# Kernel optimization log

Measured on AMD Instinct MI355X. Metric: run time of the kernel, lower is better.

## Reference

```python
import jax, jax.numpy as jnp
import numpy as np
from jax import lax

C = 256          # in_channels
CM = 16          # mid_channels = C // reduction_factor
BS = 8           # attention block size
NG = 32          # GroupNorm groups
EPS = 1e-5


def _dw(x, w, b):
    # depthwise 3x3, padding=1 -> SAME; kernel w: (C, 1, 3, 3)
    y = lax.conv_general_dilated(x, w, (1, 1), 'SAME',
                                 dimension_numbers=('NCHW', 'OIHW', 'NCHW'),
                                 feature_group_count=x.shape[1])
    return y + b[None, :, None, None]


def _pw(x, w, b):
    # pointwise 1x1 conv; w: (O, C)
    return jnp.einsum('bchw,oc->bohw', x, w) + b[None, :, None, None]


def _blocks(x, hb, wb):
    # (B, Cc, H, W) -> (B*hb*wb, Cc, BS*BS)
    B, Cc, H, W = x.shape
    x = x.reshape(B, Cc, hb, BS, wb, BS).transpose(0, 2, 4, 1, 3, 5)
    return x.reshape(B * hb * wb, Cc, BS * BS)


def _attention(q_src, k_src, v_src, p):
    B, Cin, H, W = q_src.shape
    q = _pw(_dw(q_src, p['qdw_w'], p['qdw_b']), p['qpw_w'], p['qpw_b'])  # (B,CM,H,W)
    k = _pw(_dw(k_src, p['kdw_w'], p['kdw_b']), p['kpw_w'], p['kpw_b'])  # (B,CM,H,W)
    v = _pw(_dw(v_src, p['vdw_w'], p['vdw_b']), p['vpw_w'], p['vpw_b'])  # (B,C,H,W)
    hb, wb = H // BS, W // BS  # H,W chosen divisible by BS (pad path is no-op)
    qb = _blocks(q, hb, wb)
    kb = _blocks(k, hb, wb)
    vb = _blocks(v, hb, wb)
    attn = jax.nn.softmax(jnp.einsum('ncp,ncq->npq', qb, kb) / (CM ** 0.5), axis=-1)
    out = jnp.einsum('ncq,npq->ncp', vb, attn)  # (N, C, 64)
    out = out.reshape(B, hb, wb, Cin, BS, BS).transpose(0, 3, 1, 4, 2, 5)
    return out.reshape(B, Cin, H, W)


def _group_norm(x, gamma, beta):
    B, Cc, H, W = x.shape
    xg = x.reshape(B, NG, Cc // NG, H, W)
    mu = jnp.mean(xg, axis=(2, 3, 4), keepdims=True)
    var = jnp.var(xg, axis=(2, 3, 4), keepdims=True)
    xg = (xg - mu) * lax.rsqrt(var + EPS)
    x = xg.reshape(B, Cc, H, W)
    return x * gamma[None, :, None, None] + beta[None, :, None, None]


def setup_inputs() -> dict:
    key = jax.random.key(0)
    ks = jax.random.split(key, 12)
    s = 0.05
    return {
        'img_feat': jax.random.normal(ks[0], (8, C, 128, 128), jnp.float32),
        'mask_feat': jax.random.normal(ks[1], (8, C, 128, 128), jnp.float32),
        'qdw_w': jax.random.normal(ks[2], (C, 1, 3, 3), jnp.float32) * s,
        'qdw_b': jnp.zeros((C,), jnp.float32),
        'kdw_w': jax.random.normal(ks[3], (C, 1, 3, 3), jnp.float32) * s,
        'kdw_b': jnp.zeros((C,), jnp.float32),
        'vdw_w': jax.random.normal(ks[4], (C, 1, 3, 3), jnp.float32) * s,
        'vdw_b': jnp.zeros((C,), jnp.float32),
        'qpw_w': jax.random.normal(ks[5], (CM, C), jnp.float32) * s,
        'qpw_b': jnp.zeros((CM,), jnp.float32),
        'kpw_w': jax.random.normal(ks[6], (CM, C), jnp.float32) * s,
        'kpw_b': jnp.zeros((CM,), jnp.float32),
        'vpw_w': jax.random.normal(ks[7], (C, C), jnp.float32) * s,
        'vpw_b': jnp.zeros((C,), jnp.float32),
        'alpha': jnp.float32(0.5),
        'beta': jnp.float32(0.5),
        'gn_w': jnp.ones((C,), jnp.float32),
        'gn_b': jnp.zeros((C,), jnp.float32),
    }


def reference(img_feat, mask_feat, qdw_w, qdw_b, kdw_w, kdw_b, vdw_w, vdw_b,
              qpw_w, qpw_b, kpw_w, kpw_b, vpw_w, vpw_b, alpha, beta, gn_w, gn_b):
    p = dict(qdw_w=qdw_w, qdw_b=qdw_b, kdw_w=kdw_w, kdw_b=kdw_b,
             vdw_w=vdw_w, vdw_b=vdw_b, qpw_w=qpw_w, qpw_b=qpw_b,
             kpw_w=kpw_w, kpw_b=kpw_b, vpw_w=vpw_w, vpw_b=vpw_b)
    mask_enhanced = _attention(mask_feat, img_feat, img_feat, p)
    img_enhanced = _attention(img_feat, mask_feat, mask_feat, p)
    fused = alpha * mask_enhanced + beta * img_enhanced + img_feat + mask_feat
    return _group_norm(fused, gn_w, gn_b)
```

## Files before the change

kernel.cpp:

```cpp
#include <hip/hip_runtime.h>
#include <hip/hip_bf16.h>

using bf16 = __hip_bfloat16;

typedef short s16x8 __attribute__((ext_vector_type(8)));
typedef float f32x4 __attribute__((ext_vector_type(4)));

#define TPB 512
#define MFMA16(a, b, c) __builtin_amdgcn_mfma_f32_16x16x32_bf16((a), (b), (c), 0, 0, 0)

__device__ __forceinline__ float b2f(bf16 h) { return __bfloat162float(h); }
__device__ __forceinline__ bf16  f2b(float f) { return __float2bfloat16(f); }
__device__ __forceinline__ void unpack2(unsigned int v, float& lo, float& hi) {
  lo = __builtin_bit_cast(float, v << 16);
  hi = __builtin_bit_cast(float, v & 0xffff0000u);
}
__device__ __forceinline__ void unpack8(uint4 u, float* f) {
  unpack2(u.x, f[0], f[1]); unpack2(u.y, f[2], f[3]);
  unpack2(u.z, f[4], f[5]); unpack2(u.w, f[6], f[7]);
}
__device__ __forceinline__ unsigned int pack2(float a, float b) {
  unsigned int lo = (unsigned int)__builtin_bit_cast(unsigned short, __float2bfloat16(a));
  unsigned int hi = (unsigned int)__builtin_bit_cast(unsigned short, __float2bfloat16(b));
  return lo | (hi << 16);
}
__device__ __forceinline__ s16x8 cvt8(float4 a, float4 b) {
  uint4 u;
  u.x = pack2(a.x, a.y); u.y = pack2(a.z, a.w);
  u.z = pack2(b.x, b.y); u.w = pack2(b.z, b.w);
  return __builtin_bit_cast(s16x8, u);
}

struct __align__(16) SMem {
  bf16 patch[256 * 100];
  union {
    bf16 dwT[64 * 264];
    bf16 vA[256 * 72];
    bf16 outT[256 * 72];
  } R1;
  bf16 R2[256 * 72];
  bf16 probs1[64 * 72];
  bf16 probs2[64 * 72];
  bf16 q1[16 * 64];
  bf16 k1[16 * 64];
  bf16 q2[16 * 64];
  bf16 k2[16 * 64];
  float red[2 * 8 * 64];
  float stats[64];
};

__device__ __forceinline__ void load_patch(SMem& sm, const float* __restrict__ src,
                                           int b, int by, int bx, int tid) {
  const int gx4 = bx * 8;
  for (int u = tid; u < 2560; u += TPB) {
    int c = u / 10, py = u - c * 10;
    int gy = by * 8 + py - 1;
    unsigned int* d32 = (unsigned int*)&sm.patch[c * 100 + py * 10];
    if (gy < 0 || gy > 127) {
      #pragma unroll
      for (int i = 0; i < 5; i++) d32[i] = 0u;
      continue;
    }
    const float* srow = src + (((long long)(b * 256 + c)) << 14) + ((long long)gy << 7);
    float4 t1 = *(const float4*)(srow + gx4);
    float4 t2 = *(const float4*)(srow + gx4 + 4);
    float first = (bx > 0) ? srow[gx4 - 1] : 0.0f;
    float last  = (bx < 15) ? srow[gx4 + 8] : 0.0f;
    d32[0] = pack2(first, t1.x);
    d32[1] = pack2(t1.y, t1.z);
    d32[2] = pack2(t1.w, t2.x);
    d32[3] = pack2(t2.y, t2.z);
    d32[4] = pack2(t2.w, last);
  }
}

__device__ __forceinline__ void load_prow(const bf16* p, float* r) {
  const unsigned int* q = (const unsigned int*)p;
  #pragma unroll
  for (int i = 0; i < 5; i++) unpack2(q[i], r[2 * i], r[2 * i + 1]);
}

__device__ __forceinline__ void dw_phase(SMem& sm, const float* __restrict__ w9,
                                         const float* __restrict__ bias, int tid) {
  int c = tid & 255, h = tid >> 8;
  float wr[9];
  #pragma unroll
  for (int i = 0; i < 9; i++) wr[i] = w9[c * 9 + i];
  float bs = bias[c];
  const bf16* prow = &sm.patch[c * 100];
  float r0[10], r1[10], r2[10];
  load_prow(prow + (4 * h) * 10, r0);
  load_prow(prow + (4 * h + 1) * 10, r1);
  bf16* dst = sm.R1.dwT;
  #pragma unroll
  for (int t = 0; t < 4; t++) {
    int ly = 4 * h + t;
    load_prow(prow + (ly + 2) * 10, r2);
    #pragma unroll
    for (int lx = 0; lx < 8; lx++) {
      float a = bs
        + r0[lx] * wr[0] + r0[lx + 1] * wr[1] + r0[lx + 2] * wr[2]
        + r1[lx] * wr[3] + r1[lx + 1] * wr[4] + r1[lx + 2] * wr[5]
        + r2[lx] * wr[6] + r2[lx + 1] * wr[7] + r2[lx + 2] * wr[8];
      dst[(ly * 8 + lx) * 264 + c] = f2b(a);
    }
    #pragma unroll
    for (int i = 0; i < 10; i++) { r0[i] = r1[i]; r1[i] = r2[i]; }
  }
}

__device__ __forceinline__ void pw_qk(SMem& sm, const float* __restrict__ w,
                                      const float* __restrict__ bias, bf16* dst,
                                      float scale, int tid) {
  int p = tid & 63, og = tid >> 6;
  const bf16* dwp = &sm.R1.dwT[p * 264];
  float acc0 = 0.f, acc1 = 0.f;
  #pragma unroll 4
  for (int c0 = 0; c0 < 256; c0 += 8) {
    uint4 du = *(const uint4*)(dwp + c0);
    float d[8]; unpack8(du, d);
    const float* w0 = w + og * 256 + c0;
    const float* w1 = w + (og + 8) * 256 + c0;
    float4 w0a = *(const float4*)w0, w0b = *(const float4*)(w0 + 4);
    float4 w1a = *(const float4*)w1, w1b = *(const float4*)(w1 + 4);
    acc0 += w0a.x * d[0] + w0a.y * d[1] + w0a.z * d[2] + w0a.w * d[3]
          + w0b.x * d[4] + w0b.y * d[5] + w0b.z * d[6] + w0b.w * d[7];
    acc1 += w1a.x * d[0] + w1a.y * d[1] + w1a.z * d[2] + w1a.w * d[3]
          + w1b.x * d[4] + w1b.y * d[5] + w1b.z * d[6] + w1b.w * d[7];
  }
  dst[og * 64 + p]       = f2b(scale * (acc0 + bias[og]));
  dst[(og + 8) * 64 + p] = f2b(scale * (acc1 + bias[og + 8]));
}

__device__ __forceinline__ void scores_softmax(SMem& sm, const bf16* q, const bf16* k,
                                               bf16* probs, int tid) {
  int p = tid & 63, rq = tid >> 6;
  int r0 = rq * 8;
  float s[8] = {0, 0, 0, 0, 0, 0, 0, 0};
  #pragma unroll 4
  for (int o = 0; o < 16; o++) {
    float qv = b2f(q[o * 64 + p]);
    uint4 ku = *(const uint4*)(k + o * 64 + r0);
    float kf[8]; unpack8(ku, kf);
    #pragma unroll
    for (int j = 0; j < 8; j++) s[j] += qv * kf[j];
  }
  float m = s[0];
  #pragma unroll
  for (int j = 1; j < 8; j++) m = fmaxf(m, s[j]);
  sm.red[rq * 64 + p] = m;
  __syncthreads();
  float M = sm.red[p];
  #pragma unroll
  for (int j = 1; j < 8; j++) M = fmaxf(M, sm.red[j * 64 + p]);
  float e[8], sum = 0.f;
  #pragma unroll
  for (int j = 0; j < 8; j++) { e[j] = __expf(s[j] - M); sum += e[j]; }
  sm.red[512 + rq * 64 + p] = sum;
  __syncthreads();
  float S = 0.f;
  #pragma unroll
  for (int j = 0; j < 8; j++) S += sm.red[512 + j * 64 + p];
  float inv = 1.0f / S;
  uint4 pk;
  pk.x = pack2(e[0] * inv, e[1] * inv);
  pk.y = pack2(e[2] * inv, e[3] * inv);
  pk.z = pack2(e[4] * inv, e[5] * inv);
  pk.w = pack2(e[6] * inv, e[7] * inv);
  *(uint4*)(probs + p * 72 + r0) = pk;
}

__device__ __forceinline__ void vgemm(SMem& sm, const float* __restrict__ vpw,
                                      const float* __restrict__ vpb, bf16* dstVA,
                                      float scale, int tid) {
  int lane = tid & 63, wv = tid >> 6;
  int quad = lane >> 4, l16 = lane & 15;
  int m0 = wv * 2;
  f32x4 acc[2][4];
  #pragma unroll
  for (int a = 0; a < 2; a++)
    #pragma unroll
    for (int n = 0; n < 4; n++) acc[a][n] = (f32x4){0.f, 0.f, 0.f, 0.f};
  const bf16* dwT = sm.R1.dwT;
  #pragma unroll 2
  for (int kt = 0; kt < 8; kt++) {
    int k0 = kt * 32 + quad * 8;
    const float* ar0 = vpw + (m0 * 16 + l16) * 256 + k0;
    const float* ar1 = vpw + ((m0 + 1) * 16 + l16) * 256 + k0;
    s16x8 a0 = cvt8(*(const float4*)ar0, *(const float4*)(ar0 + 4));
    s16x8 a1 = cvt8(*(const float4*)ar1, *(const float4*)(ar1 + 4));
    s16x8 bF[4];
    #pragma unroll
    for (int n = 0; n < 4; n++)
      bF[n] = __builtin_bit_cast(s16x8, *(const uint4*)(dwT + (n * 16 + l16) * 264 + k0));
    #pragma unroll
    for (int n = 0; n < 4; n++) {
      acc[0][n] = MFMA16(a0, bF[n], acc[0][n]);
      acc[1][n] = MFMA16(a1, bF[n], acc[1][n]);
    }
  }
  __syncthreads();
  #pragma unroll
  for (int a = 0; a < 2; a++) {
    #pragma unroll
    for (int i = 0; i < 4; i++) {
      int c = (m0 + a) * 16 + quad * 4 + i;
      float bs = vpb[c];
      #pragma unroll
      for (int n = 0; n < 4; n++) {
        int r = n * 16 + l16;
        dstVA[c * 72 + r] = f2b(scale * (acc[a][n][i] + bs));
      }
    }
  }
}

__device__ __forceinline__ void ogemm(const bf16* __restrict__ vA, const bf16* __restrict__ probs,
                                      f32x4 acc[2][4], int tid) {
  int lane = tid & 63, wv = tid >> 6;
  int quad = lane >> 4, l16 = lane & 15;
  int m0 = wv * 2;
  #pragma unroll
  for (int kt = 0; kt < 2; kt++) {
    int k0 = kt * 32 + quad * 8;
    s16x8 a0 = __builtin_bit_cast(s16x8, *(const uint4*)(vA + (m0 * 16 + l16) * 72 + k0));
    s16x8 a1 = __builtin_bit_cast(s16x8, *(const uint4*)(vA + ((m0 + 1) * 16 + l16) * 72 + k0));
    #pragma unroll
    for (int n = 0; n < 4; n++) {
      s16x8 bF = __builtin_bit_cast(s16x8, *(const uint4*)(probs + (n * 16 + l16) * 72 + k0));
      acc[0][n] = MFMA16(a0, bF, acc[0][n]);
      acc[1][n] = MFMA16(a1, bF, acc[1][n]);
    }
  }
}

__device__ __forceinline__ void add_center(SMem& sm, f32x4 acc[2][4], int tid) {
  int lane = tid & 63, wv = tid >> 6, quad = lane >> 4, l16 = lane & 15;
  int m0 = wv * 2;
  #pragma unroll
  for (int a = 0; a < 2; a++)
    #pragma unroll
    for (int i = 0; i < 4; i++) {
      int c = (m0 + a) * 16 + quad * 4 + i;
      const bf16* prow = &sm.patch[c * 100];
      #pragma unroll
      for (int n = 0; n < 4; n++) {
        int p = n * 16 + l16;
        int ly = p >> 3, lx = p & 7;
        acc[a][n][i] += b2f(prow[(ly + 1) * 10 + (lx + 1)]);
      }
    }
}

__global__ __launch_bounds__(TPB, 2) void bicaf_main(
    const float* __restrict__ img, const float* __restrict__ msk,
    const float* __restrict__ qdw_w, const float* __restrict__ qdw_b,
    const float* __restrict__ kdw_w, const float* __restrict__ kdw_b,
    const float* __restrict__ vdw_w, const float* __restrict__ vdw_b,
    const float* __restrict__ qpw_w, const float* __restrict__ qpw_b,
    const float* __restrict__ kpw_w, const float* __restrict__ kpw_b,
    const float* __restrict__ vpw_w, const float* __restrict__ vpw_b,
    const float* __restrict__ alphap, const float* __restrict__ betap,
    float* __restrict__ out, float* __restrict__ gstats) {
  __shared__ SMem sm;
  int tid = threadIdx.x;
  int i = blockIdx.x;
  int bx = (i >> 3) & 15;
  int gi = (i & 7) | ((i >> 7) << 3);
  int b = gi >> 4, by = gi & 15;

  if (tid < 64) sm.stats[tid] = 0.f;
  float alpha = alphap[0], beta = betap[0];

  load_patch(sm, img, b, by, bx, tid);
  __syncthreads();
  dw_phase(sm, qdw_w, qdw_b, tid); __syncthreads();
  pw_qk(sm, qpw_w, qpw_b, sm.q2, 0.25f, tid); __syncthreads();
  dw_phase(sm, kdw_w, kdw_b, tid); __syncthreads();
  pw_qk(sm, kpw_w, kpw_b, sm.k1, 1.0f, tid); __syncthreads();
  dw_phase(sm, vdw_w, vdw_b, tid); __syncthreads();
  vgemm(sm, vpw_w, vpw_b, sm.R2, alpha, tid);

  f32x4 facc[2][4];
  #pragma unroll
  for (int a = 0; a < 2; a++)
    #pragma unroll
    for (int n = 0; n < 4; n++) facc[a][n] = (f32x4){0.f, 0.f, 0.f, 0.f};
  add_center(sm, facc, tid);
  __syncthreads();

  load_patch(sm, msk, b, by, bx, tid);
  __syncthreads();
  dw_phase(sm, qdw_w, qdw_b, tid); __syncthreads();
  pw_qk(sm, qpw_w, qpw_b, sm.q1, 0.25f, tid); __syncthreads();
  dw_phase(sm, kdw_w, kdw_b, tid); __syncthreads();
  pw_qk(sm, kpw_w, kpw_b, sm.k2, 1.0f, tid); __syncthreads();
  dw_phase(sm, vdw_w, vdw_b, tid); __syncthreads();
  vgemm(sm, vpw_w, vpw_b, sm.R1.vA, beta, tid);
  __syncthreads();
  scores_softmax(sm, sm.q1, sm.k1, sm.probs1, tid); __syncthreads();
  scores_softmax(sm, sm.q2, sm.k2, sm.probs2, tid); __syncthreads();
  ogemm(sm.R1.vA, sm.probs2, facc, tid);
  ogemm(sm.R2, sm.probs1, facc, tid);
  add_center(sm, facc, tid);

  {
    int lane = tid & 63, wv = tid >> 6, quad = lane >> 4;
    int m0 = wv * 2;
    #pragma unroll
    for (int a = 0; a < 2; a++) {
      int g = (((m0 + a) * 16 + quad * 4) >> 3);
      float s = 0.f, ss = 0.f;
      #pragma unroll
      for (int n = 0; n < 4; n++)
        #pragma unroll
        for (int ii = 0; ii < 4; ii++) { float v = facc[a][n][ii]; s += v; ss += v * v; }
      atomicAdd(&sm.stats[g * 2], s);
      atomicAdd(&sm.stats[g * 2 + 1], ss);
    }
  }
  __syncthreads();

  {
    int lane = tid & 63, wv = tid >> 6, quad = lane >> 4, l16 = lane & 15;
    int m0 = wv * 2;
    #pragma unroll
    for (int a = 0; a < 2; a++)
      #pragma unroll
      for (int ii = 0; ii < 4; ii++) {
        int c = (m0 + a) * 16 + quad * 4 + ii;
        #pragma unroll
        for (int n = 0; n < 4; n++)
          sm.R1.outT[c * 72 + n * 16 + l16] = f2b(facc[a][n][ii]);
      }
  }
  __syncthreads();

  if (tid < 64) atomicAdd(&gstats[b * 64 + tid], sm.stats[tid]);

  {
    int c = tid & 255, h = tid >> 8;
    float* obase = out + (((long long)(b * 256 + c)) << 14) + (long long)(by * 8) * 128 + bx * 8;
    #pragma unroll
    for (int t = 0; t < 4; t++) {
      int ly = 4 * h + t;
      uint4 v = *(const uint4*)&sm.R1.outT[c * 72 + ly * 8];
      float f[8]; unpack8(v, f);
      *(float4*)(obase + ly * 128)     = make_float4(f[0], f[1], f[2], f[3]);
      *(float4*)(obase + ly * 128 + 4) = make_float4(f[4], f[5], f[6], f[7]);
    }
  }
}

__global__ __launch_bounds__(256) void gn_apply(float* __restrict__ out,
    const float* __restrict__ gstats, const float* __restrict__ gw,
    const float* __restrict__ gb) {
  long long idx = ((long long)blockIdx.x * 256 + threadIdx.x) * 8;
  int c = (int)((idx >> 14) & 255);
  int b = (int)(idx >> 22);
  int g = c >> 3;
  float sum = gstats[b * 64 + g * 2], ss = gstats[b * 64 + g * 2 + 1];
  const float inv_n = 1.0f / 131072.0f;
  float mean = sum * inv_n;
  float var = ss * inv_n - mean * mean;
  float rstd = rsqrtf(var + 1e-5f);
  float sc = gw[c] * rstd;
  float sh = gb[c] - mean * sc;
  float4 v0 = *(const float4*)(out + idx);
  float4 v1 = *(const float4*)(out + idx + 4);
  v0.x = v0.x * sc + sh; v0.y = v0.y * sc + sh;
  v0.z = v0.z * sc + sh; v0.w = v0.w * sc + sh;
  v1.x = v1.x * sc + sh; v1.y = v1.y * sc + sh;
  v1.z = v1.z * sc + sh; v1.w = v1.w * sc + sh;
  *(float4*)(out + idx) = v0;
  *(float4*)(out + idx + 4) = v1;
}

extern "C" void kernel_launch(void* const* d_in, const int* in_sizes, int n_in,
                              void* d_out, int out_size, void* d_ws, size_t ws_size,
                              hipStream_t stream) {
  (void)in_sizes; (void)n_in; (void)out_size; (void)ws_size;
  const float* img    = (const float*)d_in[0];
  const float* msk    = (const float*)d_in[1];
  const float* qdw_w  = (const float*)d_in[2];
  const float* qdw_b  = (const float*)d_in[3];
  const float* kdw_w  = (const float*)d_in[4];
  const float* kdw_b  = (const float*)d_in[5];
  const float* vdw_w  = (const float*)d_in[6];
  const float* vdw_b  = (const float*)d_in[7];
  const float* qpw_w  = (const float*)d_in[8];
  const float* qpw_b  = (const float*)d_in[9];
  const float* kpw_w  = (const float*)d_in[10];
  const float* kpw_b  = (const float*)d_in[11];
  const float* vpw_w  = (const float*)d_in[12];
  const float* vpw_b  = (const float*)d_in[13];
  const float* alphap = (const float*)d_in[14];
  const float* betap  = (const float*)d_in[15];
  const float* gn_w   = (const float*)d_in[16];
  const float* gn_b   = (const float*)d_in[17];
  float* out = (float*)d_out;
  float* gstats = (float*)d_ws;

  hipMemsetAsync(d_ws, 0, 2048, stream);
  bicaf_main<<<dim3(2048), dim3(TPB), 0, stream>>>(
      img, msk, qdw_w, qdw_b, kdw_w, kdw_b, vdw_w, vdw_b,
      qpw_w, qpw_b, kpw_w, kpw_b, vpw_w, vpw_b, alphap, betap, out, gstats);
  gn_apply<<<dim3(16384), dim3(256), 0, stream>>>(out, gstats, gn_w, gn_b);
}
```

Before: 972.7 us.

## Fuse GroupNorm apply into main kernel via cooperative grid sync and register stash

```diff
diff --git a/kernel.cpp b/kernel.cpp
--- a/kernel.cpp
+++ b/kernel.cpp
@@ -1,5 +1,8 @@
 #include <hip/hip_runtime.h>
 #include <hip/hip_bf16.h>
+#include <hip/hip_cooperative_groups.h>
+
+namespace cg = cooperative_groups;
 
 using bf16 = __hip_bfloat16;
 
@@ -112,7 +115,8 @@
 __device__ __forceinline__ void pw_qk(SMem& sm, const float* __restrict__ w,
                                       const float* __restrict__ bias, bf16* dst,
                                       float scale, int tid) {
-  int p = tid & 63, og = tid >> 6;
+  int p = tid & 63;
+  int og = __builtin_amdgcn_readfirstlane(tid >> 6);
   const bf16* dwp = &sm.R1.dwT[p * 264];
   float acc0 = 0.f, acc1 = 0.f;
   #pragma unroll 4
@@ -173,7 +177,8 @@
 __device__ __forceinline__ void vgemm(SMem& sm, const float* __restrict__ vpw,
                                       const float* __restrict__ vpb, bf16* dstVA,
                                       float scale, int tid) {
-  int lane = tid & 63, wv = tid >> 6;
+  int lane = tid & 63;
+  int wv = __builtin_amdgcn_readfirstlane(tid >> 6);
   int quad = lane >> 4, l16 = lane & 15;
   int m0 = wv * 2;
   f32x4 acc[2][4];
@@ -217,7 +222,8 @@
 
 __device__ __forceinline__ void ogemm(const bf16* __restrict__ vA, const bf16* __restrict__ probs,
                                       f32x4 acc[2][4], int tid) {
-  int lane = tid & 63, wv = tid >> 6;
+  int lane = tid & 63;
+  int wv = __builtin_amdgcn_readfirstlane(tid >> 6);
   int quad = lane >> 4, l16 = lane & 15;
   int m0 = wv * 2;
   #pragma unroll
@@ -252,7 +258,7 @@
     }
 }
 
-__global__ __launch_bounds__(TPB, 2) void bicaf_main(
+__global__ __launch_bounds__(TPB, 2) void bicaf_fused(
     const float* __restrict__ img, const float* __restrict__ msk,
     const float* __restrict__ qdw_w, const float* __restrict__ qdw_b,
     const float* __restrict__ kdw_w, const float* __restrict__ kdw_b,
@@ -261,119 +267,142 @@
     const float* __restrict__ kpw_w, const float* __restrict__ kpw_b,
     const float* __restrict__ vpw_w, const float* __restrict__ vpw_b,
     const float* __restrict__ alphap, const float* __restrict__ betap,
+    const float* __restrict__ gw, const float* __restrict__ gb,
     float* __restrict__ out, float* __restrict__ gstats) {
   __shared__ SMem sm;
   int tid = threadIdx.x;
-  int i = blockIdx.x;
-  int bx = (i >> 3) & 15;
-  int gi = (i & 7) | ((i >> 7) << 3);
-  int b = gi >> 4, by = gi & 15;
-
-  if (tid < 64) sm.stats[tid] = 0.f;
+  int j = blockIdx.x;
   float alpha = alphap[0], beta = betap[0];
 
-  load_patch(sm, img, b, by, bx, tid);
-  __syncthreads();
-  dw_phase(sm, qdw_w, qdw_b, tid); __syncthreads();
-  pw_qk(sm, qpw_w, qpw_b, sm.q2, 0.25f, tid); __syncthreads();
-  dw_phase(sm, kdw_w, kdw_b, tid); __syncthreads();
-  pw_qk(sm, kpw_w, kpw_b, sm.k1, 1.0f, tid); __syncthreads();
-  dw_phase(sm, vdw_w, vdw_b, tid); __syncthreads();
-  vgemm(sm, vpw_w, vpw_b, sm.R2, alpha, tid);
-
-  f32x4 facc[2][4];
-  #pragma unroll
-  for (int a = 0; a < 2; a++)
-    #pragma unroll
-    for (int n = 0; n < 4; n++) facc[a][n] = (f32x4){0.f, 0.f, 0.f, 0.f};
-  add_center(sm, facc, tid);
-  __syncthreads();
-
-  load_patch(sm, msk, b, by, bx, tid);
-  __syncthreads();
-  dw_phase(sm, qdw_w, qdw_b, tid); __syncthreads();
-  pw_qk(sm, qpw_w, qpw_b, sm.q1, 0.25f, tid); __syncthreads();
-  dw_phase(sm, kdw_w, kdw_b, tid); __syncthreads();
-  pw_qk(sm, kpw_w, kpw_b, sm.k2, 1.0f, tid); __syncthreads();
-  dw_phase(sm, vdw_w, vdw_b, tid); __syncthreads();
-  vgemm(sm, vpw_w, vpw_b, sm.R1.vA, beta, tid);
-  __syncthreads();
-  scores_softmax(sm, sm.q1, sm.k1, sm.probs1, tid); __syncthreads();
-  scores_softmax(sm, sm.q2, sm.k2, sm.probs2, tid); __syncthreads();
-  ogemm(sm.R1.vA, sm.probs2, facc, tid);
-  ogemm(sm.R2, sm.probs1, facc, tid);
-  add_center(sm, facc, tid);
+  unsigned int stash[8][16];
+
+  #pragma unroll 1
+  for (int t = 0; t < 8; ++t) {
+    int i = j + (t << 8);
+    int bx = (i >> 3) & 15;
+    int gi = (i & 7) | ((i >> 7) << 3);
+    int b = gi >> 4, by = gi & 15;
+
+    if (tid < 64) sm.stats[tid] = 0.f;
+
+    load_patch(sm, img, b, by, bx, tid);
+    __syncthreads();
+    dw_phase(sm, qdw_w, qdw_b, tid); __syncthreads();
+    pw_qk(sm, qpw_w, qpw_b, sm.q2, 0.25f, tid); __syncthreads();
+    dw_phase(sm, kdw_w, kdw_b, tid); __syncthreads();
+    pw_qk(sm, kpw_w, kpw_b, sm.k1, 1.0f, tid); __syncthreads();
+    dw_phase(sm, vdw_w, vdw_b, tid); __syncthreads();
+    vgemm(sm, vpw_w, vpw_b, sm.R2, alpha, tid);
+
+    f32x4 facc[2][4];
+    #pragma unroll
+    for (int a = 0; a < 2; a++)
+      #pragma unroll
+      for (int n = 0; n < 4; n++) facc[a][n] = (f32x4){0.f, 0.f, 0.f, 0.f};
+    add_center(sm, facc, tid);
+    __syncthreads();
+
+    load_patch(sm, msk, b, by, bx, tid);
+    __syncthreads();
+    dw_phase(sm, qdw_w, qdw_b, tid); __syncthreads();
+    pw_qk(sm, qpw_w, qpw_b, sm.q1, 0.25f, tid); __syncthreads();
+    dw_phase(sm, kdw_w, kdw_b, tid); __syncthreads();
+    pw_qk(sm, kpw_w, kpw_b, sm.k2, 1.0f, tid); __syncthreads();
+    dw_phase(sm, vdw_w, vdw_b, tid); __syncthreads();
+    vgemm(sm, vpw_w, vpw_b, sm.R1.vA, beta, tid);
+    __syncthreads();
+    scores_softmax(sm, sm.q1, sm.k1, sm.probs1, tid); __syncthreads();
+    scores_softmax(sm, sm.q2, sm.k2, sm.probs2, tid); __syncthreads();
+    ogemm(sm.R1.vA, sm.probs2, facc, tid);
+    ogemm(sm.R2, sm.probs1, facc, tid);
+    add_center(sm, facc, tid);
+
+    {
+      int lane = tid & 63, wv = tid >> 6, quad = lane >> 4;
+      int m0 = wv * 2;
+      #pragma unroll
+      for (int a = 0; a < 2; a++) {
+        int g = (((m0 + a) * 16 + quad * 4) >> 3);
+        float s = 0.f, ss = 0.f;
+        #pragma unroll
+        for (int n = 0; n < 4; n++)
+          #pragma unroll
+          for (int ii = 0; ii < 4; ii++) { float v = facc[a][n][ii]; s += v; ss += v * v; }
+        atomicAdd(&sm.stats[g * 2], s);
+        atomicAdd(&sm.stats[g * 2 + 1], ss);
+      }
+    }
+    __syncthreads();
+
+    if (tid < 64) atomicAdd(&gstats[b * 64 + tid], sm.stats[tid]);
+
+    #pragma unroll
+    for (int a = 0; a < 2; a++)
+      #pragma unroll
+      for (int n = 0; n < 4; n++) {
+        stash[t][a * 8 + n * 2 + 0] = pack2(facc[a][n][0], facc[a][n][1]);
+        stash[t][a * 8 + n * 2 + 1] = pack2(facc[a][n][2], facc[a][n][3]);
+      }
+  }
+
+  cg::this_grid().sync();
 
   {
-    int lane = tid & 63, wv = tid >> 6, quad = lane >> 4;
-    int m0 = wv * 2;
-    #pragma unroll
-    for (int a = 0; a < 2; a++) {
-      int g = (((m0 + a) * 16 + quad * 4) >> 3);
-      float s = 0.f, ss = 0.f;
-      #pragma unroll
-      for (int n = 0; n < 4; n++)
-        #pragma unroll
-        for (int ii = 0; ii < 4; ii++) { float v = facc[a][n][ii]; s += v; ss += v * v; }
-      atomicAdd(&sm.stats[g * 2], s);
-      atomicAdd(&sm.stats[g * 2 + 1], ss);
-    }
-  }
-  __syncthreads();
-
-  {
+    int c = tid & 255, h = tid >> 8;
+    float gwc = gw[c], gbc = gb[c];
     int lane = tid & 63, wv = tid >> 6, quad = lane >> 4, l16 = lane & 15;
     int m0 = wv * 2;
-    #pragma unroll
-    for (int a = 0; a < 2; a++)
-      #pragma unroll
-      for (int ii = 0; ii < 4; ii++) {
-        int c = (m0 + a) * 16 + quad * 4 + ii;
+
+    #pragma unroll 1
+    for (int t = 0; t < 8; ++t) {
+      int i = j + (t << 8);
+      int bx = (i >> 3) & 15;
+      int gi = (i & 7) | ((i >> 7) << 3);
+      int b = gi >> 4, by = gi & 15;
+
+      {
+        unsigned short* oT = (unsigned short*)sm.R1.outT;
         #pragma unroll
-        for (int n = 0; n < 4; n++)
-          sm.R1.outT[c * 72 + n * 16 + l16] = f2b(facc[a][n][ii]);
-      }
-  }
-  __syncthreads();
-
-  if (tid < 64) atomicAdd(&gstats[b * 64 + tid], sm.stats[tid]);
-
-  {
-    int c = tid & 255, h = tid >> 8;
-    float* obase = out + (((long long)(b * 256 + c)) << 14) + (long long)(by * 8) * 128 + bx * 8;
-    #pragma unroll
-    for (int t = 0; t < 4; t++) {
-      int ly = 4 * h + t;
-      uint4 v = *(const uint4*)&sm.R1.outT[c * 72 + ly * 8];
-      float f[8]; unpack8(v, f);
-      *(float4*)(obase + ly * 128)     = make_float4(f[0], f[1], f[2], f[3]);
-      *(float4*)(obase + ly * 128 + 4) = make_float4(f[4], f[5], f[6], f[7]);
-    }
-  }
-}
-
-__global__ __launch_bounds__(256) void gn_apply(float* __restrict__ out,
-    const float* __restrict__ gstats, const float* __restrict__ gw,
-    const float* __restrict__ gb) {
-  long long idx = ((long long)blockIdx.x * 256 + threadIdx.x) * 8;
-  int c = (int)((idx >> 14) & 255);
-  int b = (int)(idx >> 22);
-  int g = c >> 3;
-  float sum = gstats[b * 64 + g * 2], ss = gstats[b * 64 + g * 2 + 1];
-  const float inv_n = 1.0f / 131072.0f;
-  float mean = sum * inv_n;
-  float var = ss * inv_n - mean * mean;
-  float rstd = rsqrtf(var + 1e-5f);
-  float sc = gw[c] * rstd;
-  float sh = gb[c] - mean * sc;
-  float4 v0 = *(const float4*)(out + idx);
-  float4 v1 = *(const float4*)(out + idx + 4);
-  v0.x = v0.x * sc + sh; v0.y = v0.y * sc + sh;
-  v0.z = v0.z * sc + sh; v0.w = v0.w * sc + sh;
-  v1.x = v1.x * sc + sh; v1.y = v1.y * sc + sh;
-  v1.z = v1.z * sc + sh; v1.w = v1.w * sc + sh;
-  *(float4*)(out + idx) = v0;
-  *(float4*)(out + idx + 4) = v1;
+        for (int a = 0; a < 2; a++) {
+          int cb = (m0 + a) * 16 + quad * 4;
+          #pragma unroll
+          for (int n = 0; n < 4; n++) {
+            unsigned int d0 = stash[t][a * 8 + n * 2];
+            unsigned int d1 = stash[t][a * 8 + n * 2 + 1];
+            int col = n * 16 + l16;
+            oT[(cb + 0) * 72 + col] = (unsigned short)(d0 & 0xffffu);
+            oT[(cb + 1) * 72 + col] = (unsigned short)(d0 >> 16);
+            oT[(cb + 2) * 72 + col] = (unsigned short)(d1 & 0xffffu);
+            oT[(cb + 3) * 72 + col] = (unsigned short)(d1 >> 16);
+          }
+        }
+      }
+      __syncthreads();
+
+      {
+        int g = c >> 3;
+        float sum = gstats[b * 64 + g * 2], ssum = gstats[b * 64 + g * 2 + 1];
+        const float inv_n = 1.0f / 131072.0f;
+        float mean = sum * inv_n;
+        float var = ssum * inv_n - mean * mean;
+        float rstd = rsqrtf(var + 1e-5f);
+        float scl = gwc * rstd;
+        float sh = gbc - mean * scl;
+        float* obase = out + (((long long)(b * 256 + c)) << 14) + (long long)(by * 8) * 128 + bx * 8;
+        #pragma unroll
+        for (int r4 = 0; r4 < 4; r4++) {
+          int ly = 4 * h + r4;
+          uint4 v = *(const uint4*)&sm.R1.outT[c * 72 + ly * 8];
+          float f[8]; unpack8(v, f);
+          #pragma unroll
+          for (int q = 0; q < 8; q++) f[q] = f[q] * scl + sh;
+          *(float4*)(obase + ly * 128)     = make_float4(f[0], f[1], f[2], f[3]);
+          *(float4*)(obase + ly * 128 + 4) = make_float4(f[4], f[5], f[6], f[7]);
+        }
+      }
+      __syncthreads();
+    }
+  }
 }
 
 extern "C" void kernel_launch(void* const* d_in, const int* in_sizes, int n_in,
@@ -402,8 +431,13 @@
   float* gstats = (float*)d_ws;
 
   hipMemsetAsync(d_ws, 0, 2048, stream);
-  bicaf_main<<<dim3(2048), dim3(TPB), 0, stream>>>(
-      img, msk, qdw_w, qdw_b, kdw_w, kdw_b, vdw_w, vdw_b,
-      qpw_w, qpw_b, kpw_w, kpw_b, vpw_w, vpw_b, alphap, betap, out, gstats);
-  gn_apply<<<dim3(16384), dim3(256), 0, stream>>>(out, gstats, gn_w, gn_b);
-}
+  void* args[] = {
+    (void*)&img, (void*)&msk, (void*)&qdw_w, (void*)&qdw_b,
+    (void*)&kdw_w, (void*)&kdw_b, (void*)&vdw_w, (void*)&vdw_b,
+    (void*)&qpw_w, (void*)&qpw_b, (void*)&kpw_w, (void*)&kpw_b,
+    (void*)&vpw_w, (void*)&vpw_b, (void*)&alphap, (void*)&betap,
+    (void*)&gn_w, (void*)&gn_b, (void*)&out, (void*)&gstats
+  };
+  hipLaunchCooperativeKernel(reinterpret_cast<void*>(bicaf_fused),
+                             dim3(256), dim3(TPB), args, 0, stream);
+}
```

After: 933.1 us. 4.1% less time.

## Halve patch LDS footprint, keep V fragments in registers, persistent 4-tile blocks

Applied to the files above, without the earlier changes.

```diff
diff --git a/kernel.cpp b/kernel.cpp
--- a/kernel.cpp
+++ b/kernel.cpp
@@ -32,15 +32,15 @@
 }
 
 struct __align__(16) SMem {
-  bf16 patch[256 * 100];
+  union {
+    bf16 patchH[128 * 100];
+    struct { bf16 probs1[64 * 72]; bf16 probs2[64 * 72]; } P;
+  } U0;
   union {
     bf16 dwT[64 * 264];
     bf16 vA[256 * 72];
     bf16 outT[256 * 72];
   } R1;
-  bf16 R2[256 * 72];
-  bf16 probs1[64 * 72];
-  bf16 probs2[64 * 72];
   bf16 q1[16 * 64];
   bf16 k1[16 * 64];
   bf16 q2[16 * 64];
@@ -49,19 +49,20 @@
   float stats[64];
 };
 
-__device__ __forceinline__ void load_patch(SMem& sm, const float* __restrict__ src,
-                                           int b, int by, int bx, int tid) {
+__device__ __forceinline__ void load_patch_h(SMem& sm, const float* __restrict__ src,
+                                             int b, int by, int bx, int half, int tid) {
   const int gx4 = bx * 8;
-  for (int u = tid; u < 2560; u += TPB) {
-    int c = u / 10, py = u - c * 10;
+  for (int u = tid; u < 1280; u += TPB) {
+    int cl = u / 10, py = u - cl * 10;
     int gy = by * 8 + py - 1;
-    unsigned int* d32 = (unsigned int*)&sm.patch[c * 100 + py * 10];
+    unsigned int* d32 = (unsigned int*)&sm.U0.patchH[cl * 100 + py * 10];
     if (gy < 0 || gy > 127) {
       #pragma unroll
       for (int i = 0; i < 5; i++) d32[i] = 0u;
       continue;
     }
-    const float* srow = src + (((long long)(b * 256 + c)) << 14) + ((long long)gy << 7);
+    int cg = half * 128 + cl;
+    const float* srow = src + (((long long)(b * 256 + cg)) << 14) + ((long long)gy << 7);
     float4 t1 = *(const float4*)(srow + gx4);
     float4 t2 = *(const float4*)(srow + gx4 + 4);
     float first = (bx > 0) ? srow[gx4 - 1] : 0.0f;
@@ -80,21 +81,22 @@
   for (int i = 0; i < 5; i++) unpack2(q[i], r[2 * i], r[2 * i + 1]);
 }
 
-__device__ __forceinline__ void dw_phase(SMem& sm, const float* __restrict__ w9,
-                                         const float* __restrict__ bias, int tid) {
-  int c = tid & 255, h = tid >> 8;
+__device__ __forceinline__ void dw_phase_h(SMem& sm, const float* __restrict__ w9,
+                                           const float* __restrict__ bias, int half, int tid) {
+  int cl = tid & 127, h = tid >> 7;
+  int c = half * 128 + cl;
   float wr[9];
   #pragma unroll
   for (int i = 0; i < 9; i++) wr[i] = w9[c * 9 + i];
   float bs = bias[c];
-  const bf16* prow = &sm.patch[c * 100];
+  const bf16* prow = &sm.U0.patchH[cl * 100];
   float r0[10], r1[10], r2[10];
-  load_prow(prow + (4 * h) * 10, r0);
-  load_prow(prow + (4 * h + 1) * 10, r1);
+  load_prow(prow + (2 * h) * 10, r0);
+  load_prow(prow + (2 * h + 1) * 10, r1);
   bf16* dst = sm.R1.dwT;
   #pragma unroll
-  for (int t = 0; t < 4; t++) {
-    int ly = 4 * h + t;
+  for (int t = 0; t < 2; t++) {
+    int ly = 2 * h + t;
     load_prow(prow + (ly + 2) * 10, r2);
     #pragma unroll
     for (int lx = 0; lx < 8; lx++) {
@@ -109,14 +111,13 @@
   }
 }
 
-__device__ __forceinline__ void pw_qk(SMem& sm, const float* __restrict__ w,
-                                      const float* __restrict__ bias, bf16* dst,
-                                      float scale, int tid) {
-  int p = tid & 63, og = tid >> 6;
+__device__ __forceinline__ void pw_qk_part(SMem& sm, const float* __restrict__ w,
+                                           int cb, float& acc0, float& acc1, int tid) {
+  int p = tid & 63;
+  int og = __builtin_amdgcn_readfirstlane(tid >> 6);
   const bf16* dwp = &sm.R1.dwT[p * 264];
-  float acc0 = 0.f, acc1 = 0.f;
   #pragma unroll 4
-  for (int c0 = 0; c0 < 256; c0 += 8) {
+  for (int c0 = cb; c0 < cb + 128; c0 += 8) {
     uint4 du = *(const uint4*)(dwp + c0);
     float d[8]; unpack8(du, d);
     const float* w0 = w + og * 256 + c0;
@@ -128,6 +129,11 @@
     acc1 += w1a.x * d[0] + w1a.y * d[1] + w1a.z * d[2] + w1a.w * d[3]
           + w1b.x * d[4] + w1b.y * d[5] + w1b.z * d[6] + w1b.w * d[7];
   }
+}
+__device__ __forceinline__ void pw_qk_fin(const float* __restrict__ bias, bf16* dst,
+                                          float scale, float acc0, float acc1, int tid) {
+  int p = tid & 63;
+  int og = __builtin_amdgcn_readfirstlane(tid >> 6);
   dst[og * 64 + p]       = f2b(scale * (acc0 + bias[og]));
   dst[(og + 8) * 64 + p] = f2b(scale * (acc1 + bias[og + 8]));
 }
@@ -173,7 +179,8 @@
 __device__ __forceinline__ void vgemm(SMem& sm, const float* __restrict__ vpw,
                                       const float* __restrict__ vpb, bf16* dstVA,
                                       float scale, int tid) {
-  int lane = tid & 63, wv = tid >> 6;
+  int lane = tid & 63;
+  int wv = __builtin_amdgcn_readfirstlane(tid >> 6);
   int quad = lane >> 4, l16 = lane & 15;
   int m0 = wv * 2;
   f32x4 acc[2][4];
@@ -215,9 +222,40 @@
   }
 }
 
-__device__ __forceinline__ void ogemm(const bf16* __restrict__ vA, const bf16* __restrict__ probs,
-                                      f32x4 acc[2][4], int tid) {
-  int lane = tid & 63, wv = tid >> 6;
+__device__ __forceinline__ void load_vfrags(const bf16* __restrict__ vA, uint4 vf[2][2], int tid) {
+  int lane = tid & 63;
+  int wv = __builtin_amdgcn_readfirstlane(tid >> 6);
+  int quad = lane >> 4, l16 = lane & 15;
+  int m0 = wv * 2;
+  #pragma unroll
+  for (int kt = 0; kt < 2; kt++) {
+    int k0 = kt * 32 + quad * 8;
+    vf[kt][0] = *(const uint4*)(vA + (m0 * 16 + l16) * 72 + k0);
+    vf[kt][1] = *(const uint4*)(vA + ((m0 + 1) * 16 + l16) * 72 + k0);
+  }
+}
+
+__device__ __forceinline__ void ogemm_reg(const uint4 vf[2][2], const bf16* __restrict__ probs,
+                                          f32x4 acc[2][4], int tid) {
+  int lane = tid & 63, quad = lane >> 4, l16 = lane & 15;
+  #pragma unroll
+  for (int kt = 0; kt < 2; kt++) {
+    int k0 = kt * 32 + quad * 8;
+    s16x8 a0 = __builtin_bit_cast(s16x8, vf[kt][0]);
+    s16x8 a1 = __builtin_bit_cast(s16x8, vf[kt][1]);
+    #pragma unroll
+    for (int n = 0; n < 4; n++) {
+      s16x8 bF = __builtin_bit_cast(s16x8, *(const uint4*)(probs + (n * 16 + l16) * 72 + k0));
+      acc[0][n] = MFMA16(a0, bF, acc[0][n]);
+      acc[1][n] = MFMA16(a1, bF, acc[1][n]);
+    }
+  }
+}
+
+__device__ __forceinline__ void ogemm_lds(const bf16* __restrict__ vA, const bf16* __restrict__ probs,
+                                          f32x4 acc[2][4], int tid) {
+  int lane = tid & 63;
+  int wv = __builtin_amdgcn_readfirstlane(tid >> 6);
   int quad = lane >> 4, l16 = lane & 15;
   int m0 = wv * 2;
   #pragma unroll
@@ -234,15 +272,16 @@
   }
 }
 
-__device__ __forceinline__ void add_center(SMem& sm, f32x4 acc[2][4], int tid) {
+__device__ __forceinline__ void add_center_h(SMem& sm, f32x4 acc[2][4], int half, int tid) {
   int lane = tid & 63, wv = tid >> 6, quad = lane >> 4, l16 = lane & 15;
   int m0 = wv * 2;
   #pragma unroll
-  for (int a = 0; a < 2; a++)
+  for (int a = 0; a < 2; a++) {
+    int cb = (m0 + a) * 16 + quad * 4;
+    if ((cb >> 7) != half) continue;
     #pragma unroll
     for (int i = 0; i < 4; i++) {
-      int c = (m0 + a) * 16 + quad * 4 + i;
-      const bf16* prow = &sm.patch[c * 100];
+      const bf16* prow = &sm.U0.patchH[((cb + i) & 127) * 100];
       #pragma unroll
       for (int n = 0; n < 4; n++) {
         int p = n * 16 + l16;
@@ -250,9 +289,10 @@
         acc[a][n][i] += b2f(prow[(ly + 1) * 10 + (lx + 1)]);
       }
     }
-}
-
-__global__ __launch_bounds__(TPB, 2) void bicaf_main(
+  }
+}
+
+__global__ __launch_bounds__(TPB, 4) void bicaf_main(
     const float* __restrict__ img, const float* __restrict__ msk,
     const float* __restrict__ qdw_w, const float* __restrict__ qdw_b,
     const float* __restrict__ kdw_w, const float* __restrict__ kdw_b,
@@ -264,91 +304,119 @@
     float* __restrict__ out, float* __restrict__ gstats) {
   __shared__ SMem sm;
   int tid = threadIdx.x;
-  int i = blockIdx.x;
-  int bx = (i >> 3) & 15;
-  int gi = (i & 7) | ((i >> 7) << 3);
-  int b = gi >> 4, by = gi & 15;
-
-  if (tid < 64) sm.stats[tid] = 0.f;
+  int j = blockIdx.x;
   float alpha = alphap[0], beta = betap[0];
 
-  load_patch(sm, img, b, by, bx, tid);
-  __syncthreads();
-  dw_phase(sm, qdw_w, qdw_b, tid); __syncthreads();
-  pw_qk(sm, qpw_w, qpw_b, sm.q2, 0.25f, tid); __syncthreads();
-  dw_phase(sm, kdw_w, kdw_b, tid); __syncthreads();
-  pw_qk(sm, kpw_w, kpw_b, sm.k1, 1.0f, tid); __syncthreads();
-  dw_phase(sm, vdw_w, vdw_b, tid); __syncthreads();
-  vgemm(sm, vpw_w, vpw_b, sm.R2, alpha, tid);
-
-  f32x4 facc[2][4];
-  #pragma unroll
-  for (int a = 0; a < 2; a++)
-    #pragma unroll
-    for (int n = 0; n < 4; n++) facc[a][n] = (f32x4){0.f, 0.f, 0.f, 0.f};
-  add_center(sm, facc, tid);
-  __syncthreads();
-
-  load_patch(sm, msk, b, by, bx, tid);
-  __syncthreads();
-  dw_phase(sm, qdw_w, qdw_b, tid); __syncthreads();
-  pw_qk(sm, qpw_w, qpw_b, sm.q1, 0.25f, tid); __syncthreads();
-  dw_phase(sm, kdw_w, kdw_b, tid); __syncthreads();
-  pw_qk(sm, kpw_w, kpw_b, sm.k2, 1.0f, tid); __syncthreads();
-  dw_phase(sm, vdw_w, vdw_b, tid); __syncthreads();
-  vgemm(sm, vpw_w, vpw_b, sm.R1.vA, beta, tid);
-  __syncthreads();
-  scores_softmax(sm, sm.q1, sm.k1, sm.probs1, tid); __syncthreads();
-  scores_softmax(sm, sm.q2, sm.k2, sm.probs2, tid); __syncthreads();
-  ogemm(sm.R1.vA, sm.probs2, facc, tid);
-  ogemm(sm.R2, sm.probs1, facc, tid);
-  add_center(sm, facc, tid);
-
-  {
-    int lane = tid & 63, wv = tid >> 6, quad = lane >> 4;
-    int m0 = wv * 2;
-    #pragma unroll
-    for (int a = 0; a < 2; a++) {
-      int g = (((m0 + a) * 16 + quad * 4) >> 3);
-      float s = 0.f, ss = 0.f;
-      #pragma unroll
-      for (int n = 0; n < 4; n++)
-        #pragma unroll
-        for (int ii = 0; ii < 4; ii++) { float v = facc[a][n][ii]; s += v; ss += v * v; }
-      atomicAdd(&sm.stats[g * 2], s);
-      atomicAdd(&sm.stats[g * 2 + 1], ss);
-    }
-  }
-  __syncthreads();
-
-  {
-    int lane = tid & 63, wv = tid >> 6, quad = lane >> 4, l16 = lane & 15;
-    int m0 = wv * 2;
+  #pragma unroll 1
+  for (int t = 0; t < 4; ++t) {
+    int i = j + (t << 9);
+    int bx = (i >> 3) & 15;
+    int gi = (i & 7) | ((i >> 7) << 3);
+    int b = gi >> 4, by = gi & 15;
+
+    if (tid < 64) sm.stats[tid] = 0.f;
+
+    f32x4 facc[2][4];
     #pragma unroll
     for (int a = 0; a < 2; a++)
       #pragma unroll
-      for (int ii = 0; ii < 4; ii++) {
-        int c = (m0 + a) * 16 + quad * 4 + ii;
+      for (int n = 0; n < 4; n++) facc[a][n] = (f32x4){0.f, 0.f, 0.f, 0.f};
+
+    float qa0, qa1, ka0, ka1;
+    uint4 vf1[2][2];
+
+    load_patch_h(sm, img, b, by, bx, 0, tid); __syncthreads();
+    dw_phase_h(sm, qdw_w, qdw_b, 0, tid); add_center_h(sm, facc, 0, tid); __syncthreads();
+    qa0 = 0.f; qa1 = 0.f;
+    pw_qk_part(sm, qpw_w, 0, qa0, qa1, tid); __syncthreads();
+    dw_phase_h(sm, kdw_w, kdw_b, 0, tid); __syncthreads();
+    ka0 = 0.f; ka1 = 0.f;
+    pw_qk_part(sm, kpw_w, 0, ka0, ka1, tid); __syncthreads();
+    dw_phase_h(sm, vdw_w, vdw_b, 0, tid); __syncthreads();
+    load_patch_h(sm, img, b, by, bx, 1, tid); __syncthreads();
+    dw_phase_h(sm, qdw_w, qdw_b, 1, tid); __syncthreads();
+    pw_qk_part(sm, qpw_w, 128, qa0, qa1, tid);
+    pw_qk_fin(qpw_b, sm.q2, 0.25f, qa0, qa1, tid); __syncthreads();
+    dw_phase_h(sm, kdw_w, kdw_b, 1, tid); __syncthreads();
+    pw_qk_part(sm, kpw_w, 128, ka0, ka1, tid);
+    pw_qk_fin(kpw_b, sm.k1, 1.0f, ka0, ka1, tid); __syncthreads();
+    dw_phase_h(sm, vdw_w, vdw_b, 1, tid); add_center_h(sm, facc, 1, tid); __syncthreads();
+    vgemm(sm, vpw_w, vpw_b, sm.R1.vA, alpha, tid);
+    __syncthreads();
+    load_vfrags(sm.R1.vA, vf1, tid);
+    __syncthreads();
+
+    load_patch_h(sm, msk, b, by, bx, 0, tid); __syncthreads();
+    dw_phase_h(sm, qdw_w, qdw_b, 0, tid); add_center_h(sm, facc, 0, tid); __syncthreads();
+    qa0 = 0.f; qa1 = 0.f;
+    pw_qk_part(sm, qpw_w, 0, qa0, qa1, tid); __syncthreads();
+    dw_phase_h(sm, kdw_w, kdw_b, 0, tid); __syncthreads();
+    ka0 = 0.f; ka1 = 0.f;
+    pw_qk_part(sm, kpw_w, 0, ka0, ka1, tid); __syncthreads();
+    dw_phase_h(sm, vdw_w, vdw_b, 0, tid); __syncthreads();
+    load_patch_h(sm, msk, b, by, bx, 1, tid); __syncthreads();
+    dw_phase_h(sm, qdw_w, qdw_b, 1, tid); __syncthreads();
+    pw_qk_part(sm, qpw_w, 128, qa0, qa1, tid);
+    pw_qk_fin(qpw_b, sm.q1, 0.25f, qa0, qa1, tid); __syncthreads();
+    dw_phase_h(sm, kdw_w, kdw_b, 1, tid); __syncthreads();
+    pw_qk_part(sm, kpw_w, 128, ka0, ka1, tid);
+    pw_qk_fin(kpw_b, sm.k2, 1.0f, ka0, ka1, tid); __syncthreads();
+    dw_phase_h(sm, vdw_w, vdw_b, 1, tid); add_center_h(sm, facc, 1, tid); __syncthreads();
+    vgemm(sm, vpw_w, vpw_b, sm.R1.vA, beta, tid);
+    __syncthreads();
+
+    scores_softmax(sm, sm.q1, sm.k1, sm.U0.P.probs1, tid); __syncthreads();
+    scores_softmax(sm, sm.q2, sm.k2, sm.U0.P.probs2, tid); __syncthreads();
+    ogemm_reg(vf1, sm.U0.P.probs1, facc, tid);
+    ogemm_lds(sm.R1.vA, sm.U0.P.probs2, facc, tid);
+
+    {
+      int lane = tid & 63, wv = tid >> 6, quad = lane >> 4;
+      int m0 = wv * 2;
+      #pragma unroll
+      for (int a = 0; a < 2; a++) {
+        int g = (((m0 + a) * 16 + quad * 4) >> 3);
+        float s = 0.f, ss = 0.f;
         #pragma unroll
         for (int n = 0; n < 4; n++)
-          sm.R1.outT[c * 72 + n * 16 + l16] = f2b(facc[a][n][ii]);
+          #pragma unroll
+          for (int ii = 0; ii < 4; ii++) { float v = facc[a][n][ii]; s += v; ss += v * v; }
+        atomicAdd(&sm.stats[g * 2], s);
+        atomicAdd(&sm.stats[g * 2 + 1], ss);
       }
-  }
-  __syncthreads();
-
-  if (tid < 64) atomicAdd(&gstats[b * 64 + tid], sm.stats[tid]);
-
-  {
-    int c = tid & 255, h = tid >> 8;
-    float* obase = out + (((long long)(b * 256 + c)) << 14) + (long long)(by * 8) * 128 + bx * 8;
-    #pragma unroll
-    for (int t = 0; t < 4; t++) {
-      int ly = 4 * h + t;
-      uint4 v = *(const uint4*)&sm.R1.outT[c * 72 + ly * 8];
-      float f[8]; unpack8(v, f);
-      *(float4*)(obase + ly * 128)     = make_float4(f[0], f[1], f[2], f[3]);
-      *(float4*)(obase + ly * 128 + 4) = make_float4(f[4], f[5], f[6], f[7]);
-    }
+    }
+    __syncthreads();
+
+    if (tid < 64) atomicAdd(&gstats[b * 64 + tid], sm.stats[tid]);
+
+    {
+      int lane = tid & 63, wv = tid >> 6, quad = lane >> 4, l16 = lane & 15;
+      int m0 = wv * 2;
+      #pragma unroll
+      for (int a = 0; a < 2; a++)
+        #pragma unroll
+        for (int ii = 0; ii < 4; ii++) {
+          int c = (m0 + a) * 16 + quad * 4 + ii;
+          #pragma unroll
+          for (int n = 0; n < 4; n++)
+            sm.R1.outT[c * 72 + n * 16 + l16] = f2b(facc[a][n][ii]);
+        }
+    }
+    __syncthreads();
+
+    {
+      int c = tid & 255, h = tid >> 8;
+      float* obase = out + (((long long)(b * 256 + c)) << 14) + (long long)(by * 8) * 128 + bx * 8;
+      #pragma unroll
+      for (int t4 = 0; t4 < 4; t4++) {
+        int ly = 4 * h + t4;
+        uint4 v = *(const uint4*)&sm.R1.outT[c * 72 + ly * 8];
+        float f[8]; unpack8(v, f);
+        *(float4*)(obase + ly * 128)     = make_float4(f[0], f[1], f[2], f[3]);
+        *(float4*)(obase + ly * 128 + 4) = make_float4(f[4], f[5], f[6], f[7]);
+      }
+    }
+    __syncthreads();
   }
 }
 
@@ -402,7 +470,7 @@
   float* gstats = (float*)d_ws;
 
   hipMemsetAsync(d_ws, 0, 2048, stream);
-  bicaf_main<<<dim3(2048), dim3(TPB), 0, stream>>>(
+  bicaf_main<<<dim3(512), dim3(TPB), 0, stream>>>(
       img, msk, qdw_w, qdw_b, kdw_w, kdw_b, vdw_w, vdw_b,
       qpw_w, qpw_b, kpw_w, kpw_b, vpw_w, vpw_b, alphap, betap, out, gstats);
   gn_apply<<<dim3(16384), dim3(256), 0, stream>>>(out, gstats, gn_w, gn_b);
```

Result: faster. 872.2 us (-10.3%).
